# Kernel optimization log

Measured on AMD Instinct MI355X. Metric: run time of the kernel, lower is better.

Reference implementation:

```python
import jax, jax.numpy as jnp
import numpy as np

B, N, F, C = 8, 256, 59, 128
BOX = 20.0
EPS = 1e-5


def _bn(y, g, b, m, v):
    # eval-mode BatchNorm1d over the channel (last) axis
    return (y - m) * jax.lax.rsqrt(v + EPS) * g + b


def setup_inputs() -> dict:
    key = jax.random.key(0)
    ks = jax.random.split(key, 12)
    x = jax.random.normal(ks[0], (B, N, F), jnp.float32)
    pos = jax.random.uniform(ks[1], (B, N, 3), jnp.float32) * BOX
    nrm = jax.random.normal(ks[2], (B, N, 3), jnp.float32)
    normal = nrm / jnp.linalg.norm(nrm, axis=-1, keepdims=True)
    s_in = 1.0 / np.sqrt(F)
    W_lin = jax.random.normal(ks[3], (C, F), jnp.float32) * s_in
    W_src = jax.random.normal(ks[4], (C, F), jnp.float32) * s_in
    W_dst = jax.random.normal(ks[5], (C, F), jnp.float32) * s_in
    pos_w = jax.random.normal(ks[6], (C, 6), jnp.float32) * (1.0 / np.sqrt(6.0))
    pos_b = jax.random.normal(ks[7], (C,), jnp.float32) * 0.02
    attn_w = jax.random.normal(ks[8], (C, C), jnp.float32) * (1.0 / np.sqrt(C))
    attn_b = jax.random.normal(ks[9], (C,), jnp.float32) * 0.02
    pos_bn_g = 1.0 + 0.1 * jax.random.normal(ks[10], (C,), jnp.float32)
    attn_bn_g = 1.0 + 0.1 * jax.random.normal(ks[11], (C,), jnp.float32)
    zeros = jnp.zeros((C,), jnp.float32)
    ones = jnp.ones((C,), jnp.float32)
    return {
        'x': x, 'pos': pos, 'normal': normal,
        'W_lin': W_lin, 'W_src': W_src, 'W_dst': W_dst,
        'pos_w': pos_w, 'pos_b': pos_b,
        'pos_bn_g': pos_bn_g, 'pos_bn_b': zeros, 'pos_bn_m': zeros, 'pos_bn_v': ones,
        'attn_w': attn_w, 'attn_b': attn_b,
        'attn_bn_g': attn_bn_g, 'attn_bn_b': zeros, 'attn_bn_m': zeros, 'attn_bn_v': ones,
        'r': 5,
    }


def reference(x, pos, normal, W_lin, W_src, W_dst, pos_w, pos_b,
              pos_bn_g, pos_bn_b, pos_bn_m, pos_bn_v,
              attn_w, attn_b, attn_bn_g, attn_bn_b, attn_bn_m, attn_bn_v, r):
    r = jnp.float32(r)
    # linear projections (bias-free, as in PyG PointTransformerConv)
    v = jnp.einsum('bnf,cf->bnc', x, W_lin)      # values
    a_src = jnp.einsum('bnf,cf->bnc', x, W_src)  # alpha for source j
    a_dst = jnp.einsum('bnf,cf->bnc', x, W_dst)  # alpha for dest   i
    # relative geometry, axis 1 = receiver i, axis 2 = sender j
    rel_pos = pos[:, :, None, :] - pos[:, None, :, :]          # [B,i,j,3]
    rel_nrm = normal[:, :, None, :] - normal[:, None, :, :]    # [B,i,j,3]
    relf = jnp.concatenate([rel_pos, rel_nrm], axis=-1)        # [B,i,j,6]
    # pos_nn = Linear(6,C) + BN + ReLU (eval)
    delta = jax.nn.relu(_bn(jnp.einsum('bijk,ck->bijc', relf, pos_w) + pos_b,
                            pos_bn_g, pos_bn_b, pos_bn_m, pos_bn_v))
    # attn_nn(alpha_i - alpha_j + delta)
    alpha_arg = a_dst[:, :, None, :] - a_src[:, None, :, :] + delta
    scores = jax.nn.relu(_bn(jnp.einsum('bijc,dc->bijd', alpha_arg, attn_w) + attn_b,
                             attn_bn_g, attn_bn_b, attn_bn_m, attn_bn_v))
    # radius mask within each graph (self-loops included, dist 0 <= r)
    dist2 = jnp.sum(rel_pos * rel_pos, axis=-1)                # [B,i,j]
    mask = (dist2 <= r * r)[..., None]                         # [B,i,j,1]
    attn = jax.nn.softmax(jnp.where(mask, scores, -jnp.inf), axis=2)
    # per-channel vector attention over neighbors j: sum_j attn * (v_j + delta)
    out = jnp.sum(attn * (v[:, None, :, :] + delta), axis=2)   # [B,i,C]
    return out
```

## Files before the change

kernel.cpp:

```cpp
#include <hip/hip_runtime.h>

typedef _Float16 h2 __attribute__((ext_vector_type(2)));
typedef _Float16 f16x8 __attribute__((ext_vector_type(8)));
typedef float f32x4 __attribute__((ext_vector_type(4)));
typedef unsigned int uint32;

#define BB 8
#define NN 256
#define FF 59
#define CC 128
#define EPSV 1e-5f

#define WS_V     0
#define WS_ASRC  (WS_V + BB*NN*CC)
#define WS_ADST  (WS_ASRC + BB*NN*CC)
#define WS_PWT   (WS_ADST + BB*NN*CC)
#define WS_T1    (WS_PWT + 6*CC)
#define WS_T2    (WS_T1 + CC)
#define WS_WTB   (WS_T2 + CC)

__global__ __launch_bounds__(256) void prep_kernel(
    const float* __restrict__ x, const float* __restrict__ W_lin,
    const float* __restrict__ W_src, const float* __restrict__ W_dst,
    const float* __restrict__ pos_w, const float* __restrict__ pos_b,
    const float* __restrict__ pos_g, const float* __restrict__ pos_bb,
    const float* __restrict__ pos_m, const float* __restrict__ pos_v,
    const float* __restrict__ attn_w, const float* __restrict__ attn_b,
    const float* __restrict__ attn_g, const float* __restrict__ attn_bb,
    const float* __restrict__ attn_m, const float* __restrict__ attn_v,
    float* __restrict__ ws)
{
    int blk = blockIdx.x;
    int tid = threadIdx.x;
    if (blk < 768) {
        int type = blk >> 8;
        int g    = blk & 255;
        int b    = g >> 5;
        int n0   = (g & 31) * 8;
        const float* W = (type == 0) ? W_lin : (type == 1) ? W_src : W_dst;
        float* outp = ws + ((type == 0) ? WS_V : (type == 1) ? WS_ASRC : WS_ADST);
        __shared__ float Wl[15 * 128 * 4];
        __shared__ float xs[8 * 60];
        for (int idx = tid; idx < 15 * 128; idx += 256) {
            int f4 = idx >> 7, cc = idx & 127;
            const float* wr = W + cc * FF + f4 * 4;
            float4 wv;
            wv.x = wr[0];
            wv.y = wr[1];
            wv.z = wr[2];
            wv.w = (f4 < 14) ? wr[3] : 0.f;
            *(float4*)&Wl[idx * 4] = wv;
        }
        const float* xrow = x + (size_t)(b * NN + n0) * FF;
        for (int idx = tid; idx < 8 * 60; idx += 256) {
            int r = idx / 60, f = idx - r * 60;
            xs[idx] = (f < FF) ? xrow[r * FF + f] : 0.f;
        }
        __syncthreads();
        int c = tid & 127, h = tid >> 7;
        float acc[4];
#pragma unroll
        for (int q = 0; q < 4; ++q) acc[q] = 0.f;
#pragma unroll 3
        for (int f4 = 0; f4 < 15; ++f4) {
            float4 wq = *(const float4*)&Wl[(f4 * 128 + c) * 4];
#pragma unroll
            for (int q = 0; q < 4; ++q) {
                float4 xq = *(const float4*)&xs[(h * 4 + q) * 60 + f4 * 4];
                acc[q] = fmaf(wq.x, xq.x, acc[q]);
                acc[q] = fmaf(wq.y, xq.y, acc[q]);
                acc[q] = fmaf(wq.z, xq.z, acc[q]);
                acc[q] = fmaf(wq.w, xq.w, acc[q]);
            }
        }
#pragma unroll
        for (int q = 0; q < 4; ++q) {
            int n = n0 + h * 4 + q;
            outp[(b * NN + n) * CC + c] = acc[q];
        }
    } else {
        __shared__ float S2s[CC];
        if (tid < CC) {
            int c = tid;
            float S1 = rsqrtf(pos_v[c] + EPSV) * pos_g[c];
            ws[WS_T1 + c] = (pos_b[c] - pos_m[c]) * S1 + pos_bb[c];
#pragma unroll
            for (int k = 0; k < 6; ++k) ws[WS_PWT + k * CC + c] = pos_w[c * 6 + k] * S1;
            float S2 = rsqrtf(attn_v[c] + EPSV) * attn_g[c];
            S2s[c] = S2;
            ws[WS_T2 + c] = (attn_b[c] - attn_m[c]) * S2 + attn_bb[c];
        }
        __syncthreads();
        uint4* wtbp = (uint4*)(ws + WS_WTB);
        for (int idx = tid; idx < 32 * 64; idx += 256) {
            int l = idx & 63, ts = idx >> 6;
            int t = ts >> 2, s = ts & 3;
            int d  = t * 16 + (l & 15);
            int c0 = s * 32 + ((l >> 4) << 3);
            float S2 = S2s[d];
            float4 w0 = *(const float4*)&attn_w[d * CC + c0];
            float4 w1 = *(const float4*)&attn_w[d * CC + c0 + 4];
            h2 p0, p1, p2, p3;
            p0.x = (_Float16)(w0.x * S2); p0.y = (_Float16)(w0.y * S2);
            p1.x = (_Float16)(w0.z * S2); p1.y = (_Float16)(w0.w * S2);
            p2.x = (_Float16)(w1.x * S2); p2.y = (_Float16)(w1.y * S2);
            p3.x = (_Float16)(w1.z * S2); p3.y = (_Float16)(w1.w * S2);
            uint4 o;
            o.x = __builtin_bit_cast(uint32, p0);
            o.y = __builtin_bit_cast(uint32, p1);
            o.z = __builtin_bit_cast(uint32, p2);
            o.w = __builtin_bit_cast(uint32, p3);
            wtbp[idx] = o;
        }
    }
}

__global__ __launch_bounds__(256, 4) void main_kernel(
    const float* __restrict__ pos, const float* __restrict__ nrm,
    const int* __restrict__ rptr, const float* __restrict__ ws,
    float* __restrict__ out)
{
    const float* v    = ws + WS_V;
    const float* asrc = ws + WS_ASRC;
    const float* adst = ws + WS_ADST;
    const float* pwt  = ws + WS_PWT;
    const float* T1   = ws + WS_T1;
    const float* T2   = ws + WS_T2;

    int blk = blockIdx.x;
    int b = blk >> 8, i = blk & 255;
    int tid = threadIdx.x;

    __shared__ float relf[NN * 6];
    __shared__ int   jlist[NN];
    __shared__ int   wcnt[4];
    __shared__ int   cnt_s;
    __shared__ _Float16 alpha_h[16 * 136];
    __shared__ float    u_lds[16 * 136];

    int c    = tid & 127;
    int half = tid >> 7;
    int w    = tid >> 6;
    int lane = tid & 63;

    f16x8 bf[2][4];
    {
        const uint4* wtb = (const uint4*)(ws + WS_WTB);
#pragma unroll
        for (int tt = 0; tt < 2; ++tt)
#pragma unroll
            for (int s = 0; s < 4; ++s)
                bf[tt][s] = __builtin_bit_cast(f16x8,
                    wtb[((w * 2 + tt) * 4 + s) * 64 + lane]);
    }
    float T2a = T2[w * 32 + (lane & 15)];
    float T2b = T2[w * 32 + 16 + (lane & 15)];
    float pw[6];
#pragma unroll
    for (int k = 0; k < 6; ++k) pw[k] = pwt[k * CC + c];
    float T1c    = T1[c];
    float adst_c = adst[(b * NN + i) * CC + c];

    int rv = rptr[0];
    float r2 = (float)(rv * rv);
    const float* pib = pos + (size_t)(b * NN + i) * 3;
    const float* nib = nrm + (size_t)(b * NN + i) * 3;
    float pix = pib[0], piy = pib[1], piz = pib[2];
    float nix = nib[0], niy = nib[1], niz = nib[2];
    {
        int j = tid;
        const float* pj = pos + (size_t)(b * NN + j) * 3;
        const float* nj = nrm + (size_t)(b * NN + j) * 3;
        float dx = pix - pj[0], dy = piy - pj[1], dz = piz - pj[2];
        float ex = nix - nj[0], ey = niy - nj[1], ez = niz - nj[2];
        float d2 = dx * dx + dy * dy + dz * dz;
        bool valid = (d2 <= r2);
        unsigned long long m = __ballot(valid);
        if (lane == 0) wcnt[w] = __popcll(m);
        __syncthreads();
        int off = 0;
        for (int w2 = 0; w2 < w; ++w2) off += wcnt[w2];
        if (tid == 0) cnt_s = wcnt[0] + wcnt[1] + wcnt[2] + wcnt[3];
        int rank = __popcll(m & ((1ull << lane) - 1ull));
        if (valid) {
            int s = off + rank;
            jlist[s] = j;
            relf[s * 6 + 0] = dx; relf[s * 6 + 1] = dy; relf[s * 6 + 2] = dz;
            relf[s * 6 + 3] = ex; relf[s * 6 + 4] = ey; relf[s * 6 + 5] = ez;
        }
    }
    __syncthreads();
    int cnt = cnt_s;

    float pse0 = 0.f, pov0 = 0.f, pse1 = 0.f, pov1 = 0.f;

    for (int base = 0; base < cnt; base += 16) {
        if (base) __syncthreads();
        int tcnt = min(16, cnt - base);
#pragma unroll
        for (int q = 0; q < 8; ++q) {
            int s = 2 * q + half;
            if (s < tcnt) {
                int js = base + s;
                int j  = jlist[js];
                const float2* rp = (const float2*)&relf[js * 6];
                float2 r0 = rp[0], r1 = rp[1], r2f = rp[2];
                float dsum = T1c;
                dsum = fmaf(pw[0], r0.x, dsum);
                dsum = fmaf(pw[1], r0.y, dsum);
                dsum = fmaf(pw[2], r1.x, dsum);
                dsum = fmaf(pw[3], r1.y, dsum);
                dsum = fmaf(pw[4], r2f.x, dsum);
                dsum = fmaf(pw[5], r2f.y, dsum);
                float delta = fmaxf(dsum, 0.f);
                alpha_h[s * 136 + c] = (_Float16)(adst_c - asrc[(b * NN + j) * CC + c] + delta);
                u_lds[s * 136 + c]   = v[(b * NN + j) * CC + c] + delta;
            }
        }
        __syncthreads();
        f32x4 acc0 = {T2a, T2a, T2a, T2a};
        f32x4 acc1 = {T2b, T2b, T2b, T2b};
        {
            const _Float16* arow = &alpha_h[(lane & 15) * 136 + ((lane >> 4) << 3)];
#pragma unroll
            for (int s = 0; s < 4; ++s) {
                f16x8 af = *(const f16x8*)(arow + s * 32);
                acc0 = __builtin_amdgcn_mfma_f32_16x16x32_f16(af, bf[0][s], acc0, 0, 0, 0);
                acc1 = __builtin_amdgcn_mfma_f32_16x16x32_f16(af, bf[1][s], acc1, 0, 0, 0);
            }
        }
        {
            int d0 = w * 32 + (lane & 15);
#pragma unroll
            for (int rg = 0; rg < 4; ++rg) {
                int j = ((lane >> 4) << 2) + rg;
                if (j < tcnt) {
                    float e0 = __expf(fmaxf(acc0[rg], 0.f));
                    float e1 = __expf(fmaxf(acc1[rg], 0.f));
                    pse0 += e0;
                    pov0 += e0 * u_lds[j * 136 + d0];
                    pse1 += e1;
                    pov1 += e1 * u_lds[j * 136 + d0 + 16];
                }
            }
        }
    }

    pse0 += __shfl_xor(pse0, 16); pse0 += __shfl_xor(pse0, 32);
    pov0 += __shfl_xor(pov0, 16); pov0 += __shfl_xor(pov0, 32);
    pse1 += __shfl_xor(pse1, 16); pse1 += __shfl_xor(pse1, 32);
    pov1 += __shfl_xor(pov1, 16); pov1 += __shfl_xor(pov1, 32);
    if (lane < 16) {
        size_t o = (size_t)(b * NN + i) * CC + w * 32 + lane;
        out[o]      = pov0 / pse0;
        out[o + 16] = pov1 / pse1;
    }
}

extern "C" void kernel_launch(void* const* d_in, const int* in_sizes, int n_in,
                              void* d_out, int out_size, void* d_ws, size_t ws_size,
                              hipStream_t stream) {
    const float* x      = (const float*)d_in[0];
    const float* pos    = (const float*)d_in[1];
    const float* normal = (const float*)d_in[2];
    const float* W_lin  = (const float*)d_in[3];
    const float* W_src  = (const float*)d_in[4];
    const float* W_dst  = (const float*)d_in[5];
    const float* pos_w  = (const float*)d_in[6];
    const float* pos_b  = (const float*)d_in[7];
    const float* pos_g  = (const float*)d_in[8];
    const float* pos_bb = (const float*)d_in[9];
    const float* pos_m  = (const float*)d_in[10];
    const float* pos_v  = (const float*)d_in[11];
    const float* attn_w = (const float*)d_in[12];
    const float* attn_b = (const float*)d_in[13];
    const float* attn_g = (const float*)d_in[14];
    const float* attn_bb= (const float*)d_in[15];
    const float* attn_m = (const float*)d_in[16];
    const float* attn_v = (const float*)d_in[17];
    const int*   rptr   = (const int*)d_in[18];
    float* ws  = (float*)d_ws;
    float* out = (float*)d_out;

    prep_kernel<<<dim3(769), dim3(256), 0, stream>>>(
        x, W_lin, W_src, W_dst, pos_w, pos_b, pos_g, pos_bb, pos_m, pos_v,
        attn_w, attn_b, attn_g, attn_bb, attn_m, attn_v, ws);
    main_kernel<<<dim3(2048), dim3(256), 0, stream>>>(pos, normal, rptr, ws, out);
}
```

Baseline: 113.2 us.

## Process two receivers per block and simplify prep weight staging

Result: faster. 109.9 us (-2.9%).

```diff
diff --git a/kernel.cpp b/kernel.cpp
--- a/kernel.cpp
+++ b/kernel.cpp
@@ -39,18 +39,9 @@
         int n0   = (g & 31) * 8;
         const float* W = (type == 0) ? W_lin : (type == 1) ? W_src : W_dst;
         float* outp = ws + ((type == 0) ? WS_V : (type == 1) ? WS_ASRC : WS_ADST);
-        __shared__ float Wl[15 * 128 * 4];
+        __shared__ float Wl[CC * FF];
         __shared__ float xs[8 * 60];
-        for (int idx = tid; idx < 15 * 128; idx += 256) {
-            int f4 = idx >> 7, cc = idx & 127;
-            const float* wr = W + cc * FF + f4 * 4;
-            float4 wv;
-            wv.x = wr[0];
-            wv.y = wr[1];
-            wv.z = wr[2];
-            wv.w = (f4 < 14) ? wr[3] : 0.f;
-            *(float4*)&Wl[idx * 4] = wv;
-        }
+        for (int idx = tid; idx < CC * FF; idx += 256) Wl[idx] = W[idx];
         const float* xrow = x + (size_t)(b * NN + n0) * FF;
         for (int idx = tid; idx < 8 * 60; idx += 256) {
             int r = idx / 60, f = idx - r * 60;
@@ -58,19 +49,33 @@
         }
         __syncthreads();
         int c = tid & 127, h = tid >> 7;
+        const float* wrow = &Wl[c * FF];
         float acc[4];
 #pragma unroll
         for (int q = 0; q < 4; ++q) acc[q] = 0.f;
-#pragma unroll 3
-        for (int f4 = 0; f4 < 15; ++f4) {
-            float4 wq = *(const float4*)&Wl[(f4 * 128 + c) * 4];
+#pragma unroll 2
+        for (int f4 = 0; f4 < 14; ++f4) {
+            float w0 = wrow[f4 * 4 + 0];
+            float w1 = wrow[f4 * 4 + 1];
+            float w2 = wrow[f4 * 4 + 2];
+            float w3 = wrow[f4 * 4 + 3];
 #pragma unroll
             for (int q = 0; q < 4; ++q) {
                 float4 xq = *(const float4*)&xs[(h * 4 + q) * 60 + f4 * 4];
-                acc[q] = fmaf(wq.x, xq.x, acc[q]);
-                acc[q] = fmaf(wq.y, xq.y, acc[q]);
-                acc[q] = fmaf(wq.z, xq.z, acc[q]);
-                acc[q] = fmaf(wq.w, xq.w, acc[q]);
+                acc[q] = fmaf(w0, xq.x, acc[q]);
+                acc[q] = fmaf(w1, xq.y, acc[q]);
+                acc[q] = fmaf(w2, xq.z, acc[q]);
+                acc[q] = fmaf(w3, xq.w, acc[q]);
+            }
+        }
+        {
+            float w0 = wrow[56], w1 = wrow[57], w2 = wrow[58];
+#pragma unroll
+            for (int q = 0; q < 4; ++q) {
+                const float* xr = &xs[(h * 4 + q) * 60];
+                acc[q] = fmaf(w0, xr[56], acc[q]);
+                acc[q] = fmaf(w1, xr[57], acc[q]);
+                acc[q] = fmaf(w2, xr[58], acc[q]);
             }
         }
 #pragma unroll
@@ -128,7 +133,8 @@
     const float* T2   = ws + WS_T2;
 
     int blk = blockIdx.x;
-    int b = blk >> 8, i = blk & 255;
+    int b  = blk >> 7;
+    int i0 = (blk & 127) * 2;
     int tid = threadIdx.x;
 
     __shared__ float relf[NN * 6];
@@ -136,7 +142,7 @@
     __shared__ int   wcnt[4];
     __shared__ int   cnt_s;
     __shared__ _Float16 alpha_h[16 * 136];
-    __shared__ float    u_lds[16 * 136];
+    __shared__ float    u_lds[16 * 132];
 
     int c    = tid & 127;
     int half = tid >> 7;
@@ -158,102 +164,105 @@
     float pw[6];
 #pragma unroll
     for (int k = 0; k < 6; ++k) pw[k] = pwt[k * CC + c];
-    float T1c    = T1[c];
-    float adst_c = adst[(b * NN + i) * CC + c];
-
+    float T1c = T1[c];
     int rv = rptr[0];
     float r2 = (float)(rv * rv);
-    const float* pib = pos + (size_t)(b * NN + i) * 3;
-    const float* nib = nrm + (size_t)(b * NN + i) * 3;
-    float pix = pib[0], piy = pib[1], piz = pib[2];
-    float nix = nib[0], niy = nib[1], niz = nib[2];
-    {
-        int j = tid;
-        const float* pj = pos + (size_t)(b * NN + j) * 3;
-        const float* nj = nrm + (size_t)(b * NN + j) * 3;
-        float dx = pix - pj[0], dy = piy - pj[1], dz = piz - pj[2];
-        float ex = nix - nj[0], ey = niy - nj[1], ez = niz - nj[2];
-        float d2 = dx * dx + dy * dy + dz * dz;
-        bool valid = (d2 <= r2);
-        unsigned long long m = __ballot(valid);
-        if (lane == 0) wcnt[w] = __popcll(m);
+
+    for (int ii = 0; ii < 2; ++ii) {
+        int i = i0 + ii;
+        float adst_c = adst[(b * NN + i) * CC + c];
+        const float* pib = pos + (size_t)(b * NN + i) * 3;
+        const float* nib = nrm + (size_t)(b * NN + i) * 3;
+        float pix = pib[0], piy = pib[1], piz = pib[2];
+        float nix = nib[0], niy = nib[1], niz = nib[2];
+        {
+            int j = tid;
+            const float* pj = pos + (size_t)(b * NN + j) * 3;
+            const float* nj = nrm + (size_t)(b * NN + j) * 3;
+            float dx = pix - pj[0], dy = piy - pj[1], dz = piz - pj[2];
+            float ex = nix - nj[0], ey = niy - nj[1], ez = niz - nj[2];
+            float d2 = dx * dx + dy * dy + dz * dz;
+            bool valid = (d2 <= r2);
+            unsigned long long m = __ballot(valid);
+            if (lane == 0) wcnt[w] = __popcll(m);
+            __syncthreads();
+            int off = 0;
+            for (int w2 = 0; w2 < w; ++w2) off += wcnt[w2];
+            if (tid == 0) cnt_s = wcnt[0] + wcnt[1] + wcnt[2] + wcnt[3];
+            int rank = __popcll(m & ((1ull << lane) - 1ull));
+            if (valid) {
+                int s = off + rank;
+                jlist[s] = j;
+                relf[s * 6 + 0] = dx; relf[s * 6 + 1] = dy; relf[s * 6 + 2] = dz;
+                relf[s * 6 + 3] = ex; relf[s * 6 + 4] = ey; relf[s * 6 + 5] = ez;
+            }
+        }
         __syncthreads();
-        int off = 0;
-        for (int w2 = 0; w2 < w; ++w2) off += wcnt[w2];
-        if (tid == 0) cnt_s = wcnt[0] + wcnt[1] + wcnt[2] + wcnt[3];
-        int rank = __popcll(m & ((1ull << lane) - 1ull));
-        if (valid) {
-            int s = off + rank;
-            jlist[s] = j;
-            relf[s * 6 + 0] = dx; relf[s * 6 + 1] = dy; relf[s * 6 + 2] = dz;
-            relf[s * 6 + 3] = ex; relf[s * 6 + 4] = ey; relf[s * 6 + 5] = ez;
-        }
-    }
-    __syncthreads();
-    int cnt = cnt_s;
-
-    float pse0 = 0.f, pov0 = 0.f, pse1 = 0.f, pov1 = 0.f;
-
-    for (int base = 0; base < cnt; base += 16) {
-        if (base) __syncthreads();
-        int tcnt = min(16, cnt - base);
-#pragma unroll
-        for (int q = 0; q < 8; ++q) {
-            int s = 2 * q + half;
-            if (s < tcnt) {
-                int js = base + s;
-                int j  = jlist[js];
-                const float2* rp = (const float2*)&relf[js * 6];
-                float2 r0 = rp[0], r1 = rp[1], r2f = rp[2];
-                float dsum = T1c;
-                dsum = fmaf(pw[0], r0.x, dsum);
-                dsum = fmaf(pw[1], r0.y, dsum);
-                dsum = fmaf(pw[2], r1.x, dsum);
-                dsum = fmaf(pw[3], r1.y, dsum);
-                dsum = fmaf(pw[4], r2f.x, dsum);
-                dsum = fmaf(pw[5], r2f.y, dsum);
-                float delta = fmaxf(dsum, 0.f);
-                alpha_h[s * 136 + c] = (_Float16)(adst_c - asrc[(b * NN + j) * CC + c] + delta);
-                u_lds[s * 136 + c]   = v[(b * NN + j) * CC + c] + delta;
-            }
-        }
-        __syncthreads();
-        f32x4 acc0 = {T2a, T2a, T2a, T2a};
-        f32x4 acc1 = {T2b, T2b, T2b, T2b};
-        {
-            const _Float16* arow = &alpha_h[(lane & 15) * 136 + ((lane >> 4) << 3)];
-#pragma unroll
-            for (int s = 0; s < 4; ++s) {
-                f16x8 af = *(const f16x8*)(arow + s * 32);
-                acc0 = __builtin_amdgcn_mfma_f32_16x16x32_f16(af, bf[0][s], acc0, 0, 0, 0);
-                acc1 = __builtin_amdgcn_mfma_f32_16x16x32_f16(af, bf[1][s], acc1, 0, 0, 0);
-            }
-        }
-        {
-            int d0 = w * 32 + (lane & 15);
-#pragma unroll
-            for (int rg = 0; rg < 4; ++rg) {
-                int j = ((lane >> 4) << 2) + rg;
-                if (j < tcnt) {
-                    float e0 = __expf(fmaxf(acc0[rg], 0.f));
-                    float e1 = __expf(fmaxf(acc1[rg], 0.f));
-                    pse0 += e0;
-                    pov0 += e0 * u_lds[j * 136 + d0];
-                    pse1 += e1;
-                    pov1 += e1 * u_lds[j * 136 + d0 + 16];
+        int cnt = cnt_s;
+
+        float pse0 = 0.f, pov0 = 0.f, pse1 = 0.f, pov1 = 0.f;
+
+        for (int base = 0; base < cnt; base += 16) {
+            if (base) __syncthreads();
+            int tcnt = min(16, cnt - base);
+#pragma unroll
+            for (int q = 0; q < 8; ++q) {
+                int s = 2 * q + half;
+                if (s < tcnt) {
+                    int js = base + s;
+                    int j  = jlist[js];
+                    const float2* rp = (const float2*)&relf[js * 6];
+                    float2 r0 = rp[0], r1 = rp[1], r2f = rp[2];
+                    float dsum = T1c;
+                    dsum = fmaf(pw[0], r0.x, dsum);
+                    dsum = fmaf(pw[1], r0.y, dsum);
+                    dsum = fmaf(pw[2], r1.x, dsum);
+                    dsum = fmaf(pw[3], r1.y, dsum);
+                    dsum = fmaf(pw[4], r2f.x, dsum);
+                    dsum = fmaf(pw[5], r2f.y, dsum);
+                    float delta = fmaxf(dsum, 0.f);
+                    alpha_h[s * 136 + c] = (_Float16)(adst_c - asrc[(b * NN + j) * CC + c] + delta);
+                    u_lds[s * 132 + c]   = v[(b * NN + j) * CC + c] + delta;
                 }
             }
-        }
-    }
-
-    pse0 += __shfl_xor(pse0, 16); pse0 += __shfl_xor(pse0, 32);
-    pov0 += __shfl_xor(pov0, 16); pov0 += __shfl_xor(pov0, 32);
-    pse1 += __shfl_xor(pse1, 16); pse1 += __shfl_xor(pse1, 32);
-    pov1 += __shfl_xor(pov1, 16); pov1 += __shfl_xor(pov1, 32);
-    if (lane < 16) {
-        size_t o = (size_t)(b * NN + i) * CC + w * 32 + lane;
-        out[o]      = pov0 / pse0;
-        out[o + 16] = pov1 / pse1;
+            __syncthreads();
+            f32x4 acc0 = {T2a, T2a, T2a, T2a};
+            f32x4 acc1 = {T2b, T2b, T2b, T2b};
+            {
+                const _Float16* arow = &alpha_h[(lane & 15) * 136 + ((lane >> 4) << 3)];
+#pragma unroll
+                for (int s = 0; s < 4; ++s) {
+                    f16x8 af = *(const f16x8*)(arow + s * 32);
+                    acc0 = __builtin_amdgcn_mfma_f32_16x16x32_f16(af, bf[0][s], acc0, 0, 0, 0);
+                    acc1 = __builtin_amdgcn_mfma_f32_16x16x32_f16(af, bf[1][s], acc1, 0, 0, 0);
+                }
+            }
+            {
+                int d0 = w * 32 + (lane & 15);
+#pragma unroll
+                for (int rg = 0; rg < 4; ++rg) {
+                    int j = ((lane >> 4) << 2) + rg;
+                    if (j < tcnt) {
+                        float e0 = __expf(fmaxf(acc0[rg], 0.f));
+                        float e1 = __expf(fmaxf(acc1[rg], 0.f));
+                        pse0 += e0;
+                        pov0 += e0 * u_lds[j * 132 + d0];
+                        pse1 += e1;
+                        pov1 += e1 * u_lds[j * 132 + d0 + 16];
+                    }
+                }
+            }
+        }
+
+        pse0 += __shfl_xor(pse0, 16); pse0 += __shfl_xor(pse0, 32);
+        pov0 += __shfl_xor(pov0, 16); pov0 += __shfl_xor(pov0, 32);
+        pse1 += __shfl_xor(pse1, 16); pse1 += __shfl_xor(pse1, 32);
+        pov1 += __shfl_xor(pov1, 16); pov1 += __shfl_xor(pov1, 32);
+        if (lane < 16) {
+            size_t o = (size_t)(b * NN + i) * CC + w * 32 + lane;
+            out[o]      = pov0 / pse0;
+            out[o + 16] = pov1 / pse1;
+        }
     }
 }
 
@@ -285,5 +294,5 @@
     prep_kernel<<<dim3(769), dim3(256), 0, stream>>>(
         x, W_lin, W_src, W_dst, pos_w, pos_b, pos_g, pos_bb, pos_m, pos_v,
         attn_w, attn_b, attn_g, attn_bb, attn_m, attn_v, ws);
-    main_kernel<<<dim3(2048), dim3(256), 0, stream>>>(pos, normal, rptr, ws, out);
+    main_kernel<<<dim3(1024), dim3(256), 0, stream>>>(pos, normal, rptr, ws, out);
 }
```
